# Kernel tuning notes

Hardware: AMD Instinct MI355X
Metric: run time of the kernel (lower is better)

## Reference

```python
import jax, jax.numpy as jnp
import numpy as np

N, P, E, H = 64, 1024, 512, 8
R = E // H  # head dim


def _xavier(key, shape, dtype=jnp.float32):
    fan_in, fan_out = shape[-1], shape[-2] if len(shape) > 1 else shape[-1]
    lim = jnp.sqrt(6.0 / (fan_in + fan_out)).astype(dtype)
    return jax.random.uniform(key, shape, dtype, -lim, lim)


def setup_inputs() -> dict:
    key = jax.random.key(0)
    k1, k2, k3, k4 = jax.random.split(key, 4)
    x = jax.random.normal(k1, (N, P, E), dtype=jnp.float32)
    alpha = _xavier(k2, (H, P))          # translation-invariant attention weights
    V = _xavier(k3, (H, R, E))           # per-head value projection
    W = _xavier(k4, (E, E))              # Dense kernel
    b = jnp.zeros((E,), dtype=jnp.float32)  # Dense bias
    return {"x": x, "alpha": alpha, "V": V, "W": W, "b": b}


def _log_cosh(x):
    # log(cosh(x)) = |x| + log1p(exp(-2|x|)) - log(2), numerically stable
    ax = jnp.abs(x)
    return ax + jnp.log1p(jnp.exp(-2.0 * ax)) - jnp.log(2.0).astype(x.dtype)


def reference(x, alpha, V, W, b):
    n, p, e = x.shape
    # circulant matrix: alpha_mat[h, i, j] = alpha[h, (j - i) mod P]
    # (equivalent to stacking jnp.roll(alpha, shift=i) over i)
    idx = (jnp.arange(p)[None, :] - jnp.arange(p)[:, None]) % p  # (P, P)
    alpha_mat = alpha[:, idx]                                    # (H, P, P)
    ws = jnp.einsum('hrd,npd->nhpr', V, x)                       # (N, H, P, R)
    y = jnp.einsum('hpj,nhjr->nphr', alpha_mat, ws)              # (N, P, H, R)
    y = y.reshape(n, p, -1)                                      # (N, P, E)
    y = y @ W + b
    return _log_cosh(y)
```

## Files before the change

### kernel.cpp

```cpp
#include <hip/hip_runtime.h>
#include <math.h>

typedef float f32x4 __attribute__((ext_vector_type(4)));
typedef __bf16 bf16x8 __attribute__((ext_vector_type(8)));
typedef unsigned short u16x8 __attribute__((ext_vector_type(8)));
typedef unsigned short u16x4 __attribute__((ext_vector_type(4)));

#define LN2F_ 0.69314718055994530942f

__device__ inline unsigned short f2bf(float f) {
    unsigned u = __builtin_bit_cast(unsigned, f);
    u += 0x7fffu + ((u >> 16) & 1u);
    return (unsigned short)(u >> 16);
}

__device__ inline bf16x8 frag_ld(const unsigned short* Ls, int s, int ml, int q) {
    return __builtin_bit_cast(bf16x8,
        *(const u16x8*)(Ls + s * 512 + (((q) << 4) + (ml ^ ((q) << 1))) * 8));
}

__device__ inline void gll16(const unsigned short* g, unsigned short* l) {
    __builtin_amdgcn_global_load_lds(
        (const __attribute__((address_space(1))) unsigned int*)g,
        (__attribute__((address_space(3))) unsigned int*)l, 16, 0, 0);
}

__global__ __launch_bounds__(256) void k_cvt(const float* __restrict__ in,
                                             unsigned short* __restrict__ out, int n4) {
    int i = blockIdx.x * 256 + threadIdx.x;
    if (i >= n4) return;
    float4 v = ((const float4*)in)[i];
    u16x4 o = { f2bf(v.x), f2bf(v.y), f2bf(v.z), f2bf(v.w) };
    *(u16x4*)(out + (size_t)i * 4) = o;
}

__global__ __launch_bounds__(256) void k_build_am(const float* __restrict__ alpha,
                                                  unsigned short* __restrict__ am) {
    int t = blockIdx.x * 256 + threadIdx.x;
    int j8 = (t & 127) << 3;
    int p  = (t >> 7) & 1023;
    int h  = t >> 17;
    const float* ar = alpha + (h << 10);
    u16x8 o;
#pragma unroll
    for (int q = 0; q < 8; ++q) o[q] = f2bf(ar[(j8 + q - p) & 1023]);
    *(u16x8*)(am + ((size_t)t << 3)) = o;
}

__global__ __launch_bounds__(256) void k_build_wt(const float* __restrict__ W,
                                                  unsigned short* __restrict__ WT) {
    int t = blockIdx.x * 256 + threadIdx.x;
    int e1 = t >> 9, e = t & 511;
    WT[t] = f2bf(W[e * 512 + e1]);
}

__global__ __launch_bounds__(256) void k_gemm1(const unsigned short* __restrict__ A,
                                               const unsigned short* __restrict__ B,
                                               unsigned short* __restrict__ wsT) {
    __shared__ __align__(16) unsigned short As[128 * 32];
    __shared__ __align__(16) unsigned short Bs[128 * 32];
    const int tid = threadIdx.x;
    const int flat = blockIdx.x;
    const int xcd = flat & 7, slot = flat >> 3;
    const int m0 = (xcd * 64 + (slot >> 2)) * 128;
    const int e0 = (slot & 3) * 128;
    const int w = tid >> 6, lane = tid & 63, ml = lane & 15, quad = lane >> 4;
    const int wr = w >> 1, wc = w & 1;
    const int srl = (lane & 15) ^ ((lane >> 4) << 1);
    const int scl = lane >> 4;
    const unsigned short* pA0 = A + (size_t)(m0 + w * 32 + srl) * 512 + scl * 8;
    const unsigned short* pA1 = pA0 + 16 * 512;
    const unsigned short* pB0 = B + (size_t)(e0 + w * 32 + srl) * 512 + scl * 8;
    const unsigned short* pB1 = pB0 + 16 * 512;
    unsigned short* lA0 = As + w * 1024;
    unsigned short* lA1 = lA0 + 512;
    unsigned short* lB0 = Bs + w * 1024;
    unsigned short* lB1 = lB0 + 512;
    f32x4 acc[4][4] = {};
    for (int k0 = 0; k0 < 512; k0 += 32) {
        __syncthreads();
        gll16(pA0 + k0, lA0);
        gll16(pA1 + k0, lA1);
        gll16(pB0 + k0, lB0);
        gll16(pB1 + k0, lB1);
        __syncthreads();
        bf16x8 af[4], bfr[4];
#pragma unroll
        for (int i = 0; i < 4; ++i) {
            af[i]  = frag_ld(As, wr * 4 + i, ml, quad);
            bfr[i] = frag_ld(Bs, wc * 4 + i, ml, quad);
        }
#pragma unroll
        for (int i = 0; i < 4; ++i)
#pragma unroll
            for (int j = 0; j < 4; ++j)
                acc[i][j] = __builtin_amdgcn_mfma_f32_16x16x32_bf16(af[i], bfr[j], acc[i][j], 0, 0, 0);
    }
    const int n = m0 >> 10;
    const int pblk = m0 & 1023;
#pragma unroll
    for (int i = 0; i < 4; ++i) {
        int p = pblk + wr * 64 + i * 16 + quad * 4;
#pragma unroll
        for (int j = 0; j < 4; ++j) {
            int e = e0 + wc * 64 + j * 16 + ml;
            u16x4 o = { f2bf(acc[i][j][0]), f2bf(acc[i][j][1]),
                        f2bf(acc[i][j][2]), f2bf(acc[i][j][3]) };
            *(u16x4*)(wsT + ((size_t)n * 512 + e) * 1024 + p) = o;
        }
    }
}

__global__ __launch_bounds__(512) void k_gemm2(const unsigned short* __restrict__ wsT,
                                               const unsigned short* __restrict__ am,
                                               unsigned short* __restrict__ y) {
    __shared__ __align__(16) unsigned short As[256 * 32];
    __shared__ __align__(16) unsigned short Bs[128 * 32];
    const int tid = threadIdx.x;
    const int flat = blockIdx.x;
    const int xcd = flat & 7, slot = flat >> 3;
    const int panel = xcd * 16 + (slot >> 3);
    const int p0 = (slot & 7) * 128;
    const int h  = panel & 7;
    const int n0 = (panel >> 3) * 4;
    const int w = tid >> 6, lane = tid & 63, ml = lane & 15, quad = lane >> 4;
    const int wn = w >> 1, wp = w & 1;
    const int srl = (lane & 15) ^ ((lane >> 4) << 1);
    const int scl = lane >> 4;
    const unsigned short* pA0 = wsT + (size_t)(n0 + (w >> 1)) * 524288
        + (size_t)(h * 64 + ((2 * w) & 3) * 16 + srl) * 1024 + scl * 8;
    const unsigned short* pA1 = wsT + (size_t)(n0 + (w >> 1)) * 524288
        + (size_t)(h * 64 + ((2 * w + 1) & 3) * 16 + srl) * 1024 + scl * 8;
    const unsigned short* pB = am + ((size_t)h * 1024 + p0 + w * 16 + srl) * 1024 + scl * 8;
    unsigned short* lA0 = As + (2 * w) * 512;
    unsigned short* lA1 = lA0 + 512;
    unsigned short* lB  = Bs + w * 512;
    f32x4 acc[4][4] = {};
    for (int j0 = 0; j0 < 1024; j0 += 32) {
        __syncthreads();
        gll16(pA0 + j0, lA0);
        gll16(pA1 + j0, lA1);
        gll16(pB + j0, lB);
        __syncthreads();
        bf16x8 af[4], bfr[4];
#pragma unroll
        for (int mt = 0; mt < 4; ++mt)
            af[mt] = frag_ld(As, wn * 4 + mt, ml, quad);
#pragma unroll
        for (int nt = 0; nt < 4; ++nt)
            bfr[nt] = frag_ld(Bs, wp * 4 + nt, ml, quad);
#pragma unroll
        for (int mt = 0; mt < 4; ++mt)
#pragma unroll
            for (int nt = 0; nt < 4; ++nt)
                acc[mt][nt] = __builtin_amdgcn_mfma_f32_16x16x32_bf16(af[mt], bfr[nt], acc[mt][nt], 0, 0, 0);
    }
    const int n = n0 + wn;
#pragma unroll
    for (int mt = 0; mt < 4; ++mt) {
        int r0 = mt * 16 + quad * 4;
#pragma unroll
        for (int nt = 0; nt < 4; ++nt) {
            int p = p0 + wp * 64 + nt * 16 + ml;
            u16x4 o = { f2bf(acc[mt][nt][0]), f2bf(acc[mt][nt][1]),
                        f2bf(acc[mt][nt][2]), f2bf(acc[mt][nt][3]) };
            *(u16x4*)(y + ((size_t)n * 1024 + p) * 512 + h * 64 + r0) = o;
        }
    }
}

__global__ __launch_bounds__(256) void k_gemm3(const unsigned short* __restrict__ A,
                                               const unsigned short* __restrict__ B,
                                               const float* __restrict__ bias,
                                               float* __restrict__ out) {
    __shared__ __align__(16) unsigned short As[128 * 32];
    __shared__ __align__(16) unsigned short Bs[128 * 32];
    const int tid = threadIdx.x;
    const int flat = blockIdx.x;
    const int xcd = flat & 7, slot = flat >> 3;
    const int m0 = (xcd * 64 + (slot >> 2)) * 128;
    const int e0 = (slot & 3) * 128;
    const int w = tid >> 6, lane = tid & 63, ml = lane & 15, quad = lane >> 4;
    const int wr = w >> 1, wc = w & 1;
    const int srl = (lane & 15) ^ ((lane >> 4) << 1);
    const int scl = lane >> 4;
    const unsigned short* pA0 = A + (size_t)(m0 + w * 32 + srl) * 512 + scl * 8;
    const unsigned short* pA1 = pA0 + 16 * 512;
    const unsigned short* pB0 = B + (size_t)(e0 + w * 32 + srl) * 512 + scl * 8;
    const unsigned short* pB1 = pB0 + 16 * 512;
    unsigned short* lA0 = As + w * 1024;
    unsigned short* lA1 = lA0 + 512;
    unsigned short* lB0 = Bs + w * 1024;
    unsigned short* lB1 = lB0 + 512;
    f32x4 acc[4][4] = {};
    for (int k0 = 0; k0 < 512; k0 += 32) {
        __syncthreads();
        gll16(pA0 + k0, lA0);
        gll16(pA1 + k0, lA1);
        gll16(pB0 + k0, lB0);
        gll16(pB1 + k0, lB1);
        __syncthreads();
        bf16x8 af[4], bfr[4];
#pragma unroll
        for (int i = 0; i < 4; ++i) {
            af[i]  = frag_ld(As, wr * 4 + i, ml, quad);
            bfr[i] = frag_ld(Bs, wc * 4 + i, ml, quad);
        }
#pragma unroll
        for (int i = 0; i < 4; ++i)
#pragma unroll
            for (int j = 0; j < 4; ++j)
                acc[i][j] = __builtin_amdgcn_mfma_f32_16x16x32_bf16(af[i], bfr[j], acc[i][j], 0, 0, 0);
    }
#pragma unroll
    for (int j = 0; j < 4; ++j) {
        int e = e0 + wc * 64 + j * 16 + ml;
        float bv = bias[e];
#pragma unroll
        for (int i = 0; i < 4; ++i) {
            int mg = m0 + wr * 64 + i * 16 + quad * 4;
#pragma unroll
            for (int r = 0; r < 4; ++r) {
                float v  = acc[i][j][r] + bv;
                float ax = fabsf(v);
                float t  = __expf(-2.0f * ax);
                out[(size_t)(mg + r) * 512 + e] = ax + __logf(1.0f + t) - LN2F_;
            }
        }
    }
}

extern "C" void kernel_launch(void* const* d_in, const int* in_sizes, int n_in,
                              void* d_out, int out_size, void* d_ws, size_t ws_size,
                              hipStream_t stream) {
    const float* x     = (const float*)d_in[0];
    const float* alpha = (const float*)d_in[1];
    const float* V     = (const float*)d_in[2];
    const float* W     = (const float*)d_in[3];
    const float* b     = (const float*)d_in[4];

    unsigned short* am  = (unsigned short*)d_out;
    unsigned short* Vb  = am + 8388608;
    unsigned short* Xb  = Vb + 262144;
    unsigned short* wsT = (unsigned short*)d_ws;
    unsigned short* y   = wsT + 33554432;
    unsigned short* WT  = wsT;
    float* out = (float*)d_out;

    k_cvt<<<256, 256, 0, stream>>>(V, Vb, 65536);
    k_cvt<<<32768, 256, 0, stream>>>(x, Xb, 8388608);
    k_build_am<<<4096, 256, 0, stream>>>(alpha, am);

    k_gemm1<<<dim3(2048), 256, 0, stream>>>(Xb, Vb, wsT);
    k_gemm2<<<dim3(1024), 512, 0, stream>>>(wsT, am, y);
    k_build_wt<<<1024, 256, 0, stream>>>(W, WT);
    k_gemm3<<<dim3(2048), 256, 0, stream>>>(y, WT, b, out);
}
```

Before: 497.6 us.

## Double-buffer LDS tiles in all three GEMMs to overlap loads with MFMA

```diff
diff --git a/kernel.cpp b/kernel.cpp
--- a/kernel.cpp
+++ b/kernel.cpp
@@ -57,8 +57,8 @@
 __global__ __launch_bounds__(256) void k_gemm1(const unsigned short* __restrict__ A,
                                                const unsigned short* __restrict__ B,
                                                unsigned short* __restrict__ wsT) {
-    __shared__ __align__(16) unsigned short As[128 * 32];
-    __shared__ __align__(16) unsigned short Bs[128 * 32];
+    __shared__ __align__(16) unsigned short As[2][128 * 32];
+    __shared__ __align__(16) unsigned short Bs[2][128 * 32];
     const int tid = threadIdx.x;
     const int flat = blockIdx.x;
     const int xcd = flat & 7, slot = flat >> 3;
@@ -72,29 +72,33 @@
     const unsigned short* pA1 = pA0 + 16 * 512;
     const unsigned short* pB0 = B + (size_t)(e0 + w * 32 + srl) * 512 + scl * 8;
     const unsigned short* pB1 = pB0 + 16 * 512;
-    unsigned short* lA0 = As + w * 1024;
-    unsigned short* lA1 = lA0 + 512;
-    unsigned short* lB0 = Bs + w * 1024;
-    unsigned short* lB1 = lB0 + 512;
+    auto STAGE = [&](int b, int ko) {
+        gll16(pA0 + ko, As[b] + w * 1024);
+        gll16(pA1 + ko, As[b] + w * 1024 + 512);
+        gll16(pB0 + ko, Bs[b] + w * 1024);
+        gll16(pB1 + ko, Bs[b] + w * 1024 + 512);
+    };
     f32x4 acc[4][4] = {};
-    for (int k0 = 0; k0 < 512; k0 += 32) {
-        __syncthreads();
-        gll16(pA0 + k0, lA0);
-        gll16(pA1 + k0, lA1);
-        gll16(pB0 + k0, lB0);
-        gll16(pB1 + k0, lB1);
-        __syncthreads();
+    STAGE(0, 0);
+    __syncthreads();
+#pragma unroll 2
+    for (int k = 0; k < 16; ++k) {
+        const int cur = k & 1;
+        if (k < 15) STAGE(cur ^ 1, (k + 1) * 32);
         bf16x8 af[4], bfr[4];
 #pragma unroll
         for (int i = 0; i < 4; ++i) {
-            af[i]  = frag_ld(As, wr * 4 + i, ml, quad);
-            bfr[i] = frag_ld(Bs, wc * 4 + i, ml, quad);
-        }
+            af[i]  = frag_ld(As[cur], wr * 4 + i, ml, quad);
+            bfr[i] = frag_ld(Bs[cur], wc * 4 + i, ml, quad);
+        }
+        __builtin_amdgcn_s_setprio(1);
 #pragma unroll
         for (int i = 0; i < 4; ++i)
 #pragma unroll
             for (int j = 0; j < 4; ++j)
                 acc[i][j] = __builtin_amdgcn_mfma_f32_16x16x32_bf16(af[i], bfr[j], acc[i][j], 0, 0, 0);
+        __builtin_amdgcn_s_setprio(0);
+        __syncthreads();
     }
     const int n = m0 >> 10;
     const int pblk = m0 & 1023;
@@ -114,8 +118,8 @@
 __global__ __launch_bounds__(512) void k_gemm2(const unsigned short* __restrict__ wsT,
                                                const unsigned short* __restrict__ am,
                                                unsigned short* __restrict__ y) {
-    __shared__ __align__(16) unsigned short As[256 * 32];
-    __shared__ __align__(16) unsigned short Bs[128 * 32];
+    __shared__ __align__(16) unsigned short As[2][256 * 32];
+    __shared__ __align__(16) unsigned short Bs[2][128 * 32];
     const int tid = threadIdx.x;
     const int flat = blockIdx.x;
     const int xcd = flat & 7, slot = flat >> 3;
@@ -132,28 +136,33 @@
     const unsigned short* pA1 = wsT + (size_t)(n0 + (w >> 1)) * 524288
         + (size_t)(h * 64 + ((2 * w + 1) & 3) * 16 + srl) * 1024 + scl * 8;
     const unsigned short* pB = am + ((size_t)h * 1024 + p0 + w * 16 + srl) * 1024 + scl * 8;
-    unsigned short* lA0 = As + (2 * w) * 512;
-    unsigned short* lA1 = lA0 + 512;
-    unsigned short* lB  = Bs + w * 512;
+    auto STAGE = [&](int b, int jo) {
+        gll16(pA0 + jo, As[b] + (2 * w) * 512);
+        gll16(pA1 + jo, As[b] + (2 * w) * 512 + 512);
+        gll16(pB + jo, Bs[b] + w * 512);
+    };
     f32x4 acc[4][4] = {};
-    for (int j0 = 0; j0 < 1024; j0 += 32) {
-        __syncthreads();
-        gll16(pA0 + j0, lA0);
-        gll16(pA1 + j0, lA1);
-        gll16(pB + j0, lB);
-        __syncthreads();
+    STAGE(0, 0);
+    __syncthreads();
+#pragma unroll 2
+    for (int k = 0; k < 32; ++k) {
+        const int cur = k & 1;
+        if (k < 31) STAGE(cur ^ 1, (k + 1) * 32);
         bf16x8 af[4], bfr[4];
 #pragma unroll
         for (int mt = 0; mt < 4; ++mt)
-            af[mt] = frag_ld(As, wn * 4 + mt, ml, quad);
+            af[mt] = frag_ld(As[cur], wn * 4 + mt, ml, quad);
 #pragma unroll
         for (int nt = 0; nt < 4; ++nt)
-            bfr[nt] = frag_ld(Bs, wp * 4 + nt, ml, quad);
+            bfr[nt] = frag_ld(Bs[cur], wp * 4 + nt, ml, quad);
+        __builtin_amdgcn_s_setprio(1);
 #pragma unroll
         for (int mt = 0; mt < 4; ++mt)
 #pragma unroll
             for (int nt = 0; nt < 4; ++nt)
                 acc[mt][nt] = __builtin_amdgcn_mfma_f32_16x16x32_bf16(af[mt], bfr[nt], acc[mt][nt], 0, 0, 0);
+        __builtin_amdgcn_s_setprio(0);
+        __syncthreads();
     }
     const int n = n0 + wn;
 #pragma unroll
@@ -173,8 +182,8 @@
                                                const unsigned short* __restrict__ B,
                                                const float* __restrict__ bias,
                                                float* __restrict__ out) {
-    __shared__ __align__(16) unsigned short As[128 * 32];
-    __shared__ __align__(16) unsigned short Bs[128 * 32];
+    __shared__ __align__(16) unsigned short As[2][128 * 32];
+    __shared__ __align__(16) unsigned short Bs[2][128 * 32];
     const int tid = threadIdx.x;
     const int flat = blockIdx.x;
     const int xcd = flat & 7, slot = flat >> 3;
@@ -188,29 +197,33 @@
     const unsigned short* pA1 = pA0 + 16 * 512;
     const unsigned short* pB0 = B + (size_t)(e0 + w * 32 + srl) * 512 + scl * 8;
     const unsigned short* pB1 = pB0 + 16 * 512;
-    unsigned short* lA0 = As + w * 1024;
-    unsigned short* lA1 = lA0 + 512;
-    unsigned short* lB0 = Bs + w * 1024;
-    unsigned short* lB1 = lB0 + 512;
+    auto STAGE = [&](int b, int ko) {
+        gll16(pA0 + ko, As[b] + w * 1024);
+        gll16(pA1 + ko, As[b] + w * 1024 + 512);
+        gll16(pB0 + ko, Bs[b] + w * 1024);
+        gll16(pB1 + ko, Bs[b] + w * 1024 + 512);
+    };
     f32x4 acc[4][4] = {};
-    for (int k0 = 0; k0 < 512; k0 += 32) {
-        __syncthreads();
-        gll16(pA0 + k0, lA0);
-        gll16(pA1 + k0, lA1);
-        gll16(pB0 + k0, lB0);
-        gll16(pB1 + k0, lB1);
-        __syncthreads();
+    STAGE(0, 0);
+    __syncthreads();
+#pragma unroll 2
+    for (int k = 0; k < 16; ++k) {
+        const int cur = k & 1;
+        if (k < 15) STAGE(cur ^ 1, (k + 1) * 32);
         bf16x8 af[4], bfr[4];
 #pragma unroll
         for (int i = 0; i < 4; ++i) {
-            af[i]  = frag_ld(As, wr * 4 + i, ml, quad);
-            bfr[i] = frag_ld(Bs, wc * 4 + i, ml, quad);
-        }
+            af[i]  = frag_ld(As[cur], wr * 4 + i, ml, quad);
+            bfr[i] = frag_ld(Bs[cur], wc * 4 + i, ml, quad);
+        }
+        __builtin_amdgcn_s_setprio(1);
 #pragma unroll
         for (int i = 0; i < 4; ++i)
 #pragma unroll
             for (int j = 0; j < 4; ++j)
                 acc[i][j] = __builtin_amdgcn_mfma_f32_16x16x32_bf16(af[i], bfr[j], acc[i][j], 0, 0, 0);
+        __builtin_amdgcn_s_setprio(0);
+        __syncthreads();
     }
 #pragma unroll
     for (int j = 0; j < 4; ++j) {
```

Result: no change. 500.9 us (+0.7%).
